# Performance work log

Measured on AMD Instinct MI355X. Metric: run time of the kernel, lower is better.

## Reference

```python
import jax, jax.numpy as jnp
import numpy as np

EMBED = 512
HEADS = 8
HEAD_LEN = EMBED // HEADS  # 64


def setup_inputs() -> dict:
    key = jax.random.key(0)
    ks = jax.random.split(key, 8)
    B, L = 8, 2048
    return {
        "query": jax.random.normal(ks[0], (B, L, EMBED), dtype=jnp.float32),
        "key": jax.random.normal(ks[1], (B, L, EMBED), dtype=jnp.float32),
        "value": jax.random.normal(ks[2], (B, L, EMBED), dtype=jnp.float32),
        "Wq": jax.random.normal(ks[3], (HEAD_LEN, HEAD_LEN), dtype=jnp.float32) * 0.05,
        "Wk": jax.random.normal(ks[4], (HEAD_LEN, HEAD_LEN), dtype=jnp.float32) * 0.05,
        "Wv": jax.random.normal(ks[5], (HEAD_LEN, HEAD_LEN), dtype=jnp.float32) * 0.05,
        "Wo": jax.random.normal(ks[6], (EMBED, EMBED), dtype=jnp.float32) * 0.05,
        "bo": jax.random.normal(ks[7], (EMBED,), dtype=jnp.float32) * 0.05,
    }


def reference(query, key, value, Wq, Wk, Wv, Wo, bo):
    B, Lq, E = query.shape
    Lk = key.shape[1]
    Lv = value.shape[1]
    H, d = HEADS, HEAD_LEN
    # Faithful to original: q/k reshaped to (B, H, L, d) (splits the sequence
    # dim, not the feature dim); v reshaped to (B, L, H, d).
    q = query.reshape(B, H, Lq, d) @ Wq.T   # nn.Linear: x @ W^T
    k = key.reshape(B, H, Lk, d) @ Wk.T
    v = value.reshape(B, Lv, H, d) @ Wv.T
    scores = jnp.einsum('bhqf,bhkf->bhqk', q, k) / (E ** 0.5)  # scale = sqrt(embed_size)
    w = jax.nn.softmax(scores, axis=3)
    out = jnp.einsum('bhql,blhd->bqhd', w, v).reshape(B, Lq, H * d)
    return out @ Wo.T + bo
```

## Files before the change

kernel.cpp:

```cpp
#include <hip/hip_runtime.h>
#include <stdint.h>

#define BB 8
#define LL 2048
#define EE 512
#define HH 8
#define DD 64

typedef __attribute__((ext_vector_type(8))) short short8;
typedef __attribute__((ext_vector_type(4))) float f32x4;
typedef __attribute__((ext_vector_type(16))) float f32x16;
typedef __attribute__((ext_vector_type(2))) unsigned int u32x2v;

#define QSCALE 0.06376435773361453f

__device__ __forceinline__ uint32_t pk2bf(float a, float b) {
    union { float f; uint32_t u; } va, vb; va.f = a; vb.f = b;
    return __builtin_amdgcn_perm(vb.u + 0x8000u, va.u + 0x8000u, 0x07060302u);
}

__device__ __forceinline__ short8 pack8(const float4 t0, const float4 t1) {
    union { uint32_t u[4]; short8 s; } r;
    r.u[0] = pk2bf(t0.x, t0.y); r.u[1] = pk2bf(t0.z, t0.w);
    r.u[2] = pk2bf(t1.x, t1.y); r.u[3] = pk2bf(t1.z, t1.w);
    return r.s;
}

__global__ __launch_bounds__(256) void prep_weights(const float* __restrict__ Wq, const float* __restrict__ Wk,
                                                    const float* __restrict__ Wv, const float* __restrict__ Wo,
                                                    short* __restrict__ WqB, short* __restrict__ WkB,
                                                    short* __restrict__ WvB, short* __restrict__ WoB) {
    int i = blockIdx.x * 256 + threadIdx.x;
    const float* src; short* dst; int off;
    if (i < 1024)      { src = Wq; dst = WqB; off = i; }
    else if (i < 2048) { src = Wk; dst = WkB; off = i - 1024; }
    else if (i < 3072) { src = Wv; dst = WvB; off = i - 2048; }
    else               { src = Wo; dst = WoB; off = i - 3072; }
    float4 t = reinterpret_cast<const float4*>(src)[off];
    uint2 d; d.x = pk2bf(t.x, t.y); d.y = pk2bf(t.z, t.w);
    reinterpret_cast<uint2*>(dst)[off] = d;
}

__global__ __launch_bounds__(256) void proj_fused(const float* __restrict__ query, const float* __restrict__ key,
                                                  const float* __restrict__ value,
                                                  const short* __restrict__ WqB, const short* __restrict__ WkB,
                                                  const short* __restrict__ WvB,
                                                  short* __restrict__ Oq, short* __restrict__ Ok, short* __restrict__ OvT) {
    const int id = blockIdx.x;
    const int lane = threadIdx.x & 63;
    const int wave = threadIdx.x >> 6;
    const int quad = lane >> 4;
    const int c    = lane & 15;

    if (id < 4096) {
        const bool isq = id < 2048;
        const float* X = isq ? query : key;
        const short* W = isq ? WqB : WkB;
        short* O = isq ? Oq : Ok;
        const float oscale = isq ? QSCALE : 1.0f;
        const int xid = isq ? id : id - 2048;
        const long r0 = (long)xid * 64 + wave * 16;

        short8 xb[2];
#pragma unroll
        for (int kk = 0; kk < 2; ++kk) {
            const float* src = X + (r0 + c) * 64 + kk * 32 + quad * 8;
            xb[kk] = pack8(*reinterpret_cast<const float4*>(src), *reinterpret_cast<const float4*>(src + 4));
        }

        f32x4 acc[4];
#pragma unroll
        for (int ft = 0; ft < 4; ++ft) { acc[ft][0]=0.f; acc[ft][1]=0.f; acc[ft][2]=0.f; acc[ft][3]=0.f; }

#pragma unroll
        for (int ft = 0; ft < 4; ++ft)
#pragma unroll
            for (int kk = 0; kk < 2; ++kk) {
                short8 wa = *reinterpret_cast<const short8*>(W + (ft * 16 + c) * 64 + kk * 32 + quad * 8);
                acc[ft] = __builtin_amdgcn_mfma_f32_16x16x32_bf16(wa, xb[kk], acc[ft], 0, 0, 0);
            }

#pragma unroll
        for (int ft = 0; ft < 4; ++ft) {
            uint2 d;
            d.x = pk2bf(acc[ft][0] * oscale, acc[ft][1] * oscale);
            d.y = pk2bf(acc[ft][2] * oscale, acc[ft][3] * oscale);
            *reinterpret_cast<uint2*>(O + (r0 + c) * 64 + ft * 16 + quad * 4) = d;
        }
    } else {
        const int vid = id - 4096;
        const int bh = vid >> 5, lt = vid & 31;
        const int b = bh >> 3, h = bh & 7;
        const int l0 = lt * 64 + wave * 16;

        short8 xa[2];
#pragma unroll
        for (int kk = 0; kk < 2; ++kk) {
            const float* src = value + ((long)(b * LL + l0 + c) * EE + h * 64) + kk * 32 + quad * 8;
            xa[kk] = pack8(*reinterpret_cast<const float4*>(src), *reinterpret_cast<const float4*>(src + 4));
        }

        f32x4 acc[4];
#pragma unroll
        for (int nt = 0; nt < 4; ++nt) { acc[nt][0]=0.f; acc[nt][1]=0.f; acc[nt][2]=0.f; acc[nt][3]=0.f; }

#pragma unroll
        for (int nt = 0; nt < 4; ++nt)
#pragma unroll
            for (int kk = 0; kk < 2; ++kk) {
                short8 wb = *reinterpret_cast<const short8*>(WvB + (nt * 16 + c) * 64 + kk * 32 + quad * 8);
                acc[nt] = __builtin_amdgcn_mfma_f32_16x16x32_bf16(xa[kk], wb, acc[nt], 0, 0, 0);
            }

#pragma unroll
        for (int nt = 0; nt < 4; ++nt) {
            uint2 d;
            d.x = pk2bf(acc[nt][0], acc[nt][1]);
            d.y = pk2bf(acc[nt][2], acc[nt][3]);
            *reinterpret_cast<uint2*>(OvT + ((long)bh * 64 + nt * 16 + c) * LL + l0 + quad * 4) = d;
        }
    }
}

#define TILE(kf, vfr) { \
    _Pragma("unroll") for (int t = 0; t < 2; ++t) \
    _Pragma("unroll") for (int kt = 0; kt < 2; ++kt) { \
        f32x16 s; \
        _Pragma("unroll") for (int i = 0; i < 16; ++i) s[i] = 0.f; \
        _Pragma("unroll") for (int ks = 0; ks < 4; ++ks) \
            s = __builtin_amdgcn_mfma_f32_32x32x16_bf16(kf[kt][ks], aq[t][ks], s, 0, 0, 0); \
        uint32_t xd[4][2]; float lac = 0.f; \
        _Pragma("unroll") for (int g = 0; g < 4; ++g) { \
            const float p0 = __builtin_amdgcn_exp2f(s[4 * g + 0]); \
            const float p1 = __builtin_amdgcn_exp2f(s[4 * g + 1]); \
            const float p2 = __builtin_amdgcn_exp2f(s[4 * g + 2]); \
            const float p3 = __builtin_amdgcn_exp2f(s[4 * g + 3]); \
            lac += (p0 + p1) + (p2 + p3); \
            xd[g][0] = pk2bf(p0, p1); xd[g][1] = pk2bf(p2, p3); \
        } \
        l[t] += lac; \
        _Pragma("unroll") for (int kt2 = 0; kt2 < 2; ++kt2) { \
            u32x2v rA = __builtin_amdgcn_permlane32_swap(xd[2 * kt2][0], xd[2 * kt2 + 1][0], false, false); \
            u32x2v rB = __builtin_amdgcn_permlane32_swap(xd[2 * kt2][1], xd[2 * kt2 + 1][1], false, false); \
            union { uint32_t u[4]; short8 s8; } pb; \
            pb.u[0] = rA[0]; pb.u[1] = rB[0]; pb.u[2] = rA[1]; pb.u[3] = rB[1]; \
            const int kk = kt * 2 + kt2; \
            of[t][0] = __builtin_amdgcn_mfma_f32_32x32x16_bf16(vfr[0][kk], pb.s8, of[t][0], 0, 0, 0); \
            of[t][1] = __builtin_amdgcn_mfma_f32_32x32x16_bf16(vfr[1][kk], pb.s8, of[t][1], 0, 0, 0); \
        } \
    } }

__global__ __launch_bounds__(256, 2) void attn_kernel(const short* __restrict__ Q, const short* __restrict__ K,
                                                      const short* __restrict__ VT, short* __restrict__ Oattn) {
    __shared__ __align__(16) char smem[2][16384];
    const int lane = threadIdx.x & 63;
    const int wave = threadIdx.x >> 6;
    const int hl = lane >> 5;
    const int c  = lane & 31;
    const int bh = blockIdx.x & 63;
    const int qs = blockIdx.x >> 6;
    const int b = bh >> 3, head = bh & 7;
    const int q0 = qs * 256 + wave * 64;

    const short* Kb = K  + (long)bh * LL * 64;
    const short* Vb = VT + (long)bh * 64 * LL;

    const int wr = wave * 4096 + ((lane * 16) ^ (((lane >> 3) & 7) << 4));
    const char* sbase;
    long sstep, kbmul;
    if (wave < 2) {
        sbase = (const char*)Kb + wave * 4096 + lane * 16;
        sstep = 1024; kbmul = 128;
    } else {
        sbase = (const char*)Vb + ((long)((wave - 2) * 32 + (lane >> 3))) * 4096 + (lane & 7) * 16;
        sstep = 8 * 4096; kbmul = 2;
    }

    const int swzl = (c & 7) << 4;

    short8 aq[2][4];
#pragma unroll
    for (int t = 0; t < 2; ++t)
#pragma unroll
        for (int ks = 0; ks < 4; ++ks)
            aq[t][ks] = *reinterpret_cast<const short8*>(Q + ((long)bh * LL + q0 + t * 32 + c) * 64 + ks * 16 + hl * 8);

    f32x16 of[2][2];
#pragma unroll
    for (int t = 0; t < 2; ++t)
#pragma unroll
        for (int ft = 0; ft < 2; ++ft)
#pragma unroll
            for (int i = 0; i < 16; ++i) of[t][ft][i] = 0.f;
    float l[2] = {0.f, 0.f};

    {
        uint4 st[4];
#pragma unroll
        for (int j = 0; j < 4; ++j) st[j] = *reinterpret_cast<const uint4*>(sbase + j * sstep);
#pragma unroll
        for (int j = 0; j < 4; ++j) *reinterpret_cast<uint4*>(&smem[0][wr + j * 1024]) = st[j];
    }
    __syncthreads();

    int cur = 0;
#pragma unroll 1
    for (int kb = 0; kb < LL; kb += 64) {
        uint4 st[4];
        const long nkb = (kb + 64) & (LL - 1);
#pragma unroll
        for (int j = 0; j < 4; ++j) st[j] = *reinterpret_cast<const uint4*>(sbase + j * sstep + nkb * kbmul);

        short8 kf[2][4], vf[2][4];
        {
            const char* bp = &smem[cur][0];
#pragma unroll
            for (int kt_ = 0; kt_ < 2; ++kt_)
#pragma unroll
                for (int ks_ = 0; ks_ < 4; ++ks_)
                    kf[kt_][ks_] = *reinterpret_cast<const short8*>(bp + (kt_ * 32 + c) * 128 + ((ks_ * 32 + hl * 16) ^ swzl));
#pragma unroll
            for (int ft_ = 0; ft_ < 2; ++ft_)
#pragma unroll
                for (int kk_ = 0; kk_ < 4; ++kk_)
                    vf[ft_][kk_] = *reinterpret_cast<const short8*>(bp + 8192 + (ft_ * 32 + c) * 128 + ((kk_ * 32 + hl * 16) ^ swzl));
        }
        TILE(kf, vf);

#pragma unroll
        for (int j = 0; j < 4; ++j) *reinterpret_cast<uint4*>(&smem[cur ^ 1][wr + j * 1024]) = st[j];
        __syncthreads();
        cur ^= 1;
    }

    float inv[2];
#pragma unroll
    for (int t = 0; t < 2; ++t) {
        l[t] += __shfl_xor(l[t], 32);
        inv[t] = 1.0f / l[t];
    }

#pragma unroll
    for (int t = 0; t < 2; ++t) {
        const long row = (long)b * LL + q0 + t * 32 + c;
#pragma unroll
        for (int ft = 0; ft < 2; ++ft)
#pragma unroll
            for (int g = 0; g < 4; ++g) {
                const float v0 = of[t][ft][4 * g + 0] * inv[t], v1 = of[t][ft][4 * g + 1] * inv[t];
                const float v2 = of[t][ft][4 * g + 2] * inv[t], v3 = of[t][ft][4 * g + 3] * inv[t];
                uint2 d; d.x = pk2bf(v0, v1); d.y = pk2bf(v2, v3);
                *reinterpret_cast<uint2*>(Oattn + row * EE + head * 64 + ft * 32 + g * 8 + hl * 4) = d;
            }
    }
}

__global__ __launch_bounds__(256) void out_proj(const short* __restrict__ A, const short* __restrict__ WoB,
                                                const float* __restrict__ bo, float* __restrict__ out) {
    const int lane = threadIdx.x & 63;
    const int wave = threadIdx.x >> 6;
    const int quad = lane >> 4;
    const int c    = lane & 15;
    const int nb = blockIdx.x;
    const int rb = blockIdx.y;
    const long r0 = (long)rb * 64 + wave * 16;

    f32x4 acc[4];
#pragma unroll
    for (int ft = 0; ft < 4; ++ft) { acc[ft][0]=0.f; acc[ft][1]=0.f; acc[ft][2]=0.f; acc[ft][3]=0.f; }

    for (int ks = 0; ks < 16; ++ks) {
        short8 bfr = *reinterpret_cast<const short8*>(A + (r0 + c) * EE + ks * 32 + quad * 8);
#pragma unroll
        for (int ft = 0; ft < 4; ++ft) {
            short8 afr = *reinterpret_cast<const short8*>(WoB + ((long)(nb * 64 + ft * 16 + c)) * EE + ks * 32 + quad * 8);
            acc[ft] = __builtin_amdgcn_mfma_f32_16x16x32_bf16(afr, bfr, acc[ft], 0, 0, 0);
        }
    }

#pragma unroll
    for (int ft = 0; ft < 4; ++ft) {
        float4 bias = *reinterpret_cast<const float4*>(bo + nb * 64 + ft * 16 + quad * 4);
        float4 res;
        res.x = acc[ft][0] + bias.x; res.y = acc[ft][1] + bias.y;
        res.z = acc[ft][2] + bias.z; res.w = acc[ft][3] + bias.w;
        *reinterpret_cast<float4*>(out + (r0 + c) * EE + nb * 64 + ft * 16 + quad * 4) = res;
    }
}

extern "C" void kernel_launch(void* const* d_in, const int* in_sizes, int n_in,
                              void* d_out, int out_size, void* d_ws, size_t ws_size,
                              hipStream_t stream) {
    const float* query = (const float*)d_in[0];
    const float* key   = (const float*)d_in[1];
    const float* value = (const float*)d_in[2];
    const float* Wq    = (const float*)d_in[3];
    const float* Wk    = (const float*)d_in[4];
    const float* Wv    = (const float*)d_in[5];
    const float* Wo    = (const float*)d_in[6];
    const float* bo    = (const float*)d_in[7];
    float* out = (float*)d_out;

    char* ws = (char*)d_ws;
    const size_t SZ = 16777216;
    short* q_ws    = (short*)(ws);
    short* k_ws    = (short*)(ws + SZ);
    short* vT_ws   = (short*)(ws + 2 * SZ);
    short* attn_ws = (short*)(ws + 3 * SZ);
    short* wo_ws   = (short*)(ws + 4 * SZ);
    short* wq_ws   = (short*)(ws + 4 * SZ + 524288);
    short* wk_ws   = (short*)(ws + 4 * SZ + 532480);
    short* wv_ws   = (short*)(ws + 4 * SZ + 540672);

    prep_weights<<<268, 256, 0, stream>>>(Wq, Wk, Wv, Wo, wq_ws, wk_ws, wv_ws, wo_ws);
    proj_fused<<<6144, 256, 0, stream>>>(query, key, value, wq_ws, wk_ws, wv_ws, q_ws, k_ws, vT_ws);
    attn_kernel<<<512, 256, 0, stream>>>(q_ws, k_ws, vT_ws, attn_ws);
    out_proj<<<dim3(8, 256), 256, 0, stream>>>(attn_ws, wo_ws, bo, out);
}
```

Baseline: 318.7 us.

## Split attention key range in two and merge partials in a combine kernel

The attention kernel now splits the 2048-key loop into two halves, doubling the grid from 512 to 1024 blocks. Each block writes its unnormalized partial output as bf16 plus its per-row softmax denominators. A new combine kernel then adds the two partials and divides by the summed denominators before the output projection. The aim is more parallelism and better CU load balance, at the cost of an extra kernel launch, about 48 MB of extra global traffic, and bf16 rounding of the unnormalized partials.

```diff
diff --git a/kernel.cpp b/kernel.cpp
--- a/kernel.cpp
+++ b/kernel.cpp
@@ -24,6 +24,13 @@
     r.u[0] = pk2bf(t0.x, t0.y); r.u[1] = pk2bf(t0.z, t0.w);
     r.u[2] = pk2bf(t1.x, t1.y); r.u[3] = pk2bf(t1.z, t1.w);
     return r.s;
+}
+
+__device__ __forceinline__ float bf_lo(uint32_t u) {
+    union { uint32_t u; float f; } v; v.u = u << 16; return v.f;
+}
+__device__ __forceinline__ float bf_hi(uint32_t u) {
+    union { uint32_t u; float f; } v; v.u = u & 0xffff0000u; return v.f;
 }
 
 __global__ __launch_bounds__(256) void prep_weights(const float* __restrict__ Wq, const float* __restrict__ Wk,
@@ -151,14 +158,16 @@
     } }
 
 __global__ __launch_bounds__(256, 2) void attn_kernel(const short* __restrict__ Q, const short* __restrict__ K,
-                                                      const short* __restrict__ VT, short* __restrict__ Oattn) {
+                                                      const short* __restrict__ VT, short* __restrict__ Opart,
+                                                      float* __restrict__ lws) {
     __shared__ __align__(16) char smem[2][16384];
     const int lane = threadIdx.x & 63;
     const int wave = threadIdx.x >> 6;
     const int hl = lane >> 5;
     const int c  = lane & 31;
     const int bh = blockIdx.x & 63;
-    const int qs = blockIdx.x >> 6;
+    const int qs = (blockIdx.x >> 6) & 7;
+    const int split = blockIdx.x >> 9;
     const int b = bh >> 3, head = bh & 7;
     const int q0 = qs * 256 + wave * 64;
 
@@ -194,10 +203,12 @@
             for (int i = 0; i < 16; ++i) of[t][ft][i] = 0.f;
     float l[2] = {0.f, 0.f};
 
+    const int kb0 = split * 1024;
+
     {
         uint4 st[4];
 #pragma unroll
-        for (int j = 0; j < 4; ++j) st[j] = *reinterpret_cast<const uint4*>(sbase + j * sstep);
+        for (int j = 0; j < 4; ++j) st[j] = *reinterpret_cast<const uint4*>(sbase + j * sstep + (long)kb0 * kbmul);
 #pragma unroll
         for (int j = 0; j < 4; ++j) *reinterpret_cast<uint4*>(&smem[0][wr + j * 1024]) = st[j];
     }
@@ -205,9 +216,9 @@
 
     int cur = 0;
 #pragma unroll 1
-    for (int kb = 0; kb < LL; kb += 64) {
+    for (int kb = kb0; kb < kb0 + 1024; kb += 64) {
         uint4 st[4];
-        const long nkb = (kb + 64) & (LL - 1);
+        const long nkb = kb0 + ((kb - kb0 + 64) & 1023);
 #pragma unroll
         for (int j = 0; j < 4; ++j) st[j] = *reinterpret_cast<const uint4*>(sbase + j * sstep + nkb * kbmul);
 
@@ -233,13 +244,15 @@
         cur ^= 1;
     }
 
-    float inv[2];
-#pragma unroll
-    for (int t = 0; t < 2; ++t) {
-        l[t] += __shfl_xor(l[t], 32);
-        inv[t] = 1.0f / l[t];
-    }
-
+#pragma unroll
+    for (int t = 0; t < 2; ++t) l[t] += __shfl_xor(l[t], 32);
+    if (hl == 0) {
+        float* lp = lws + (long)split * (64 * LL) + bh * LL + q0;
+        lp[c] = l[0];
+        lp[32 + c] = l[1];
+    }
+
+    short* Od = Opart + (long)split * (BB * LL * EE);
 #pragma unroll
     for (int t = 0; t < 2; ++t) {
         const long row = (long)b * LL + q0 + t * 32 + c;
@@ -247,12 +260,35 @@
         for (int ft = 0; ft < 2; ++ft)
 #pragma unroll
             for (int g = 0; g < 4; ++g) {
-                const float v0 = of[t][ft][4 * g + 0] * inv[t], v1 = of[t][ft][4 * g + 1] * inv[t];
-                const float v2 = of[t][ft][4 * g + 2] * inv[t], v3 = of[t][ft][4 * g + 3] * inv[t];
-                uint2 d; d.x = pk2bf(v0, v1); d.y = pk2bf(v2, v3);
-                *reinterpret_cast<uint2*>(Oattn + row * EE + head * 64 + ft * 32 + g * 8 + hl * 4) = d;
+                uint2 d;
+                d.x = pk2bf(of[t][ft][4 * g + 0], of[t][ft][4 * g + 1]);
+                d.y = pk2bf(of[t][ft][4 * g + 2], of[t][ft][4 * g + 3]);
+                *reinterpret_cast<uint2*>(Od + row * EE + head * 64 + ft * 32 + g * 8 + hl * 4) = d;
             }
     }
+}
+
+__global__ __launch_bounds__(256) void combine_attn(const short* __restrict__ Opart, const float* __restrict__ lws,
+                                                    short* __restrict__ Oattn) {
+    const int g = blockIdx.x * 256 + threadIdx.x;
+    const int row = g >> 6;
+    const int f0  = (g & 63) * 8;
+    const int bh  = ((row >> 11) << 3) + (f0 >> 6);
+    const int rl  = row & (LL - 1);
+    const float l0 = lws[(long)bh * LL + rl];
+    const float l1 = lws[(long)64 * LL + (long)bh * LL + rl];
+    const float inv = 1.0f / (l0 + l1);
+
+    union { short8 s; uint32_t u[4]; } x0, x1, o;
+    x0.s = reinterpret_cast<const short8*>(Opart)[g];
+    x1.s = reinterpret_cast<const short8*>(Opart + (long)BB * LL * EE)[g];
+#pragma unroll
+    for (int d = 0; d < 4; ++d) {
+        const float lo = bf_lo(x0.u[d]) + bf_lo(x1.u[d]);
+        const float hi = bf_hi(x0.u[d]) + bf_hi(x1.u[d]);
+        o.u[d] = pk2bf(lo * inv, hi * inv);
+    }
+    reinterpret_cast<short8*>(Oattn)[g] = o.s;
 }
 
 __global__ __launch_bounds__(256) void out_proj(const short* __restrict__ A, const short* __restrict__ WoB,
@@ -306,14 +342,17 @@
     short* q_ws    = (short*)(ws);
     short* k_ws    = (short*)(ws + SZ);
     short* vT_ws   = (short*)(ws + 2 * SZ);
-    short* attn_ws = (short*)(ws + 3 * SZ);
-    short* wo_ws   = (short*)(ws + 4 * SZ);
-    short* wq_ws   = (short*)(ws + 4 * SZ + 524288);
-    short* wk_ws   = (short*)(ws + 4 * SZ + 532480);
-    short* wv_ws   = (short*)(ws + 4 * SZ + 540672);
+    short* op_ws   = (short*)(ws + 3 * SZ);
+    float* l_ws    = (float*)(ws + 5 * SZ);
+    short* attn_ws = q_ws;
+    short* wo_ws   = (short*)(ws + 5 * SZ + 2097152);
+    short* wq_ws   = (short*)(ws + 5 * SZ + 2097152 + 524288);
+    short* wk_ws   = (short*)(ws + 5 * SZ + 2097152 + 532480);
+    short* wv_ws   = (short*)(ws + 5 * SZ + 2097152 + 540672);
 
     prep_weights<<<268, 256, 0, stream>>>(Wq, Wk, Wv, Wo, wq_ws, wk_ws, wv_ws, wo_ws);
     proj_fused<<<6144, 256, 0, stream>>>(query, key, value, wq_ws, wk_ws, wv_ws, q_ws, k_ws, vT_ws);
-    attn_kernel<<<512, 256, 0, stream>>>(q_ws, k_ws, vT_ws, attn_ws);
+    attn_kernel<<<1024, 256, 0, stream>>>(q_ws, k_ws, vT_ws, op_ws, l_ws);
+    combine_attn<<<4096, 256, 0, stream>>>(op_ws, l_ws, attn_ws);
     out_proj<<<dim3(8, 256), 256, 0, stream>>>(attn_ws, wo_ws, bo, out);
 }
```

New measurement: 329.3 us. +3.3%, slower.
